# Kernel tuning notes

Hardware: AMD Instinct MI355X
Metric: run time of the kernel (lower is better)

Reference implementation:

```python
import jax, jax.numpy as jnp
import numpy as np

EPS = 1e-8


def setup_inputs() -> dict:
    key = jax.random.key(0)
    ks = jax.random.split(key, 8)
    B, N, D = 8, 2048, 768
    H, R = 768, 4
    return {
        "x": jax.random.normal(ks[0], (B, N, D), dtype=jnp.float32),
        "scale": jnp.ones((D,), dtype=jnp.float32),
        "U": jax.random.normal(ks[1], (H, R), dtype=jnp.float32) * 0.02,
        "V": jax.random.normal(ks[2], (H, R), dtype=jnp.float32) * 0.02,
        "S_param": jax.random.normal(ks[3], (H, H), dtype=jnp.float32) * 0.01,
        "Bm": jax.random.normal(ks[4], (H, D), dtype=jnp.float32) * (1.0 / np.sqrt(D)),
        "Cm": jax.random.normal(ks[5], (D, H), dtype=jnp.float32) * (1.0 / np.sqrt(H)),
        "gate_w": jax.random.normal(ks[6], (D, D), dtype=jnp.float32) * (1.0 / np.sqrt(D)),
        "gate_b": jnp.zeros((D,), dtype=jnp.float32),
        "alpha": jnp.full((1,), 0.1, dtype=jnp.float32),
    }


def reference(x, scale, U, V, S_param, Bm, Cm, gate_w, gate_b, alpha):
    B, N, D = x.shape
    H = Bm.shape[0]
    # A = diag(A_diag) + U V^T + (S - S^T); A_diag is a fixed buffer.
    A_diag = -jnp.linspace(1.0, float(H), H, dtype=x.dtype) / H
    A = jnp.diag(A_diag) + U @ V.T + (S_param - S_param.T)
    At = A.T  # apply as h @ A.T
    # RMSNorm
    rms = jnp.sqrt(jnp.mean(x * x, axis=-1, keepdims=True) + EPS)
    xn = x / rms * scale
    # Precompute input injections u_t = x_t @ B.T for all t: (N, B, H)
    u = jnp.einsum('bnd,hd->nbh', xn, Bm)

    def step(h, ut):
        h = h @ At + ut
        return h, h @ Cm.T  # (B, D)

    h0 = jnp.zeros((B, H), dtype=x.dtype)
    _, y_fwd = jax.lax.scan(step, h0, u)                 # (N, B, D)
    _, y_bwd = jax.lax.scan(step, h0, u, reverse=True)   # (N, B, D), indexed in time order
    y = 0.5 * (y_fwd + y_bwd)
    y = jnp.swapaxes(y, 0, 1)  # (B, N, D)
    # Gate
    g = jax.nn.sigmoid(jnp.einsum('bnd,ed->bne', xn, gate_w) + gate_b)
    y = y * g
    # Skip (dropout is identity in eval)
    return x + alpha * y
```

## Files before the change

kernel.cpp:

```cpp
#include <hip/hip_runtime.h>


typedef short  bfrag __attribute__((ext_vector_type(8)));
typedef float  ffrag __attribute__((ext_vector_type(4)));
typedef float  f4    __attribute__((ext_vector_type(4)));
typedef short  s4v   __attribute__((ext_vector_type(4)));

#define DEV static __device__ __forceinline__
#define Hn 768

DEV unsigned short f2bf(float f) {
  unsigned u = __float_as_uint(f);
  u += 0x7fffu + ((u >> 16) & 1u);
  return (unsigned short)(u >> 16);
}
DEV float bf2f(unsigned short s) { return __uint_as_float(((unsigned)s) << 16); }

DEV ffrag mfma16(bfrag a, bfrag b, ffrag c) {
  return __builtin_amdgcn_mfma_f32_16x16x32_bf16(a, b, c, 0, 0, 0);
}

DEV void glds16(const unsigned short* g, unsigned short* l) {
  __builtin_amdgcn_global_load_lds(
      (const __attribute__((address_space(1))) unsigned int*)g,
      (__attribute__((address_space(3))) unsigned int*)l, 16, 0, 0);
}

union BF8 { bfrag v; unsigned short u[8]; };

__global__ __launch_bounds__(256) void k_abuild(
    const float* __restrict__ U, const float* __restrict__ V,
    const float* __restrict__ S, const float* __restrict__ Bm,
    const float* __restrict__ Cm, const float* __restrict__ gw,
    float* __restrict__ Af, float* __restrict__ AfT,
    unsigned short* __restrict__ Abf,
    unsigned short* __restrict__ Bmb, unsigned short* __restrict__ Cmb,
    unsigned short* __restrict__ gwb, unsigned short* __restrict__ zp) {
  int i = blockIdx.x;
  int task = blockIdx.y;
  if (task == 0) {
    float u0 = U[i*4+0], u1 = U[i*4+1], u2 = U[i*4+2], u3 = U[i*4+3];
    for (int j = threadIdx.x; j < Hn; j += 256) {
      float a = u0*V[j*4+0] + u1*V[j*4+1] + u2*V[j*4+2] + u3*V[j*4+3]
              + S[i*Hn+j] - S[j*Hn+i];
      if (i == j) a += -(float)(i+1) / 768.0f;
      Af[i*Hn+j]  = a;
      AfT[j*Hn+i] = a;
      Abf[i*Hn+j] = f2bf(a);
    }
    if (i == 0) for (int j = threadIdx.x; j < 1024; j += 256) zp[j] = 0;
  } else {
    const float* src = (task==1) ? Bm : (task==2) ? Cm : gw;
    unsigned short* dst = (task==1) ? Bmb : (task==2) ? Cmb : gwb;
    for (int j = threadIdx.x; j < Hn; j += 256) dst[i*Hn+j] = f2bf(src[i*Hn+j]);
  }
}

__global__ __launch_bounds__(256) void k_rms(
    const float* __restrict__ x, const float* __restrict__ scale,
    unsigned short* __restrict__ xn) {
  int row  = blockIdx.x * 4 + (threadIdx.x >> 6);
  int lane = threadIdx.x & 63;
  int b = row >> 11, t = row & 2047;
  const float* xr = x + (long)row * Hn;
  float v[12];
  float ss = 0.f;
#pragma unroll
  for (int j = 0; j < 12; ++j) { v[j] = xr[lane + j*64]; ss += v[j]*v[j]; }
#pragma unroll
  for (int off = 1; off < 64; off <<= 1) ss += __shfl_xor(ss, off);
  float inv = 1.0f / sqrtf(ss / 768.0f + 1e-8f);
  unsigned short* dst = xn + ((long)t * 8 + b) * Hn;
#pragma unroll
  for (int j = 0; j < 12; ++j) dst[lane + j*64] = f2bf(v[j] * inv * scale[lane + j*64]);
}

__global__ __launch_bounds__(512) void k_sq(
    const float* __restrict__ X, const float* __restrict__ XT,
    float* __restrict__ Z, float* __restrict__ ZT,
    unsigned short* __restrict__ Zbf) {
  int tid = threadIdx.x, lane = tid & 63, w = tid >> 6;
  int mw = w >> 2, nw = w & 3, l15 = lane & 15, lhi = lane >> 4;
  int rb = blockIdx.x * 64, cb = blockIdx.y * 128;
  ffrag acc[2][2] = {};
  for (int kt = 0; kt < 24; ++kt) {
    int k0 = kt*32 + lhi*8;
    BF8 ah[2], al[2], bh[2], bl[2];
#pragma unroll
    for (int mt = 0; mt < 2; ++mt) {
      const f4* p = (const f4*)(X + (long)(rb + mw*32 + mt*16 + l15) * Hn + k0);
      f4 x0 = p[0], x1 = p[1];
#pragma unroll
      for (int j = 0; j < 8; ++j) {
        float f = (j < 4) ? x0[j] : x1[j-4];
        unsigned short h = f2bf(f);
        ah[mt].u[j] = h; al[mt].u[j] = f2bf(f - bf2f(h));
      }
    }
#pragma unroll
    for (int nt = 0; nt < 2; ++nt) {
      const f4* p = (const f4*)(XT + (long)(cb + nw*32 + nt*16 + l15) * Hn + k0);
      f4 x0 = p[0], x1 = p[1];
#pragma unroll
      for (int j = 0; j < 8; ++j) {
        float f = (j < 4) ? x0[j] : x1[j-4];
        unsigned short h = f2bf(f);
        bh[nt].u[j] = h; bl[nt].u[j] = f2bf(f - bf2f(h));
      }
    }
#pragma unroll
    for (int mt = 0; mt < 2; ++mt)
#pragma unroll
      for (int nt = 0; nt < 2; ++nt) {
        acc[mt][nt] = mfma16(ah[mt].v, bh[nt].v, acc[mt][nt]);
        acc[mt][nt] = mfma16(ah[mt].v, bl[nt].v, acc[mt][nt]);
        acc[mt][nt] = mfma16(al[mt].v, bh[nt].v, acc[mt][nt]);
      }
  }
#pragma unroll
  for (int mt = 0; mt < 2; ++mt)
#pragma unroll
    for (int nt = 0; nt < 2; ++nt)
#pragma unroll
      for (int q = 0; q < 4; ++q) {
        int grow = rb + mw*32 + mt*16 + lhi*4 + q;
        int gcol = cb + nw*32 + nt*16 + l15;
        float vv = acc[mt][nt][q];
        Z[(long)grow*Hn + gcol] = vv;
        ZT[(long)gcol*Hn + grow] = vv;
        Zbf[(long)grow*Hn + gcol] = f2bf(vv);
      }
}

template<int MODE>
__global__ __launch_bounds__(256) void k_gemm(
    const unsigned short* __restrict__ A0s, const unsigned short* __restrict__ B0s,
    const unsigned short* __restrict__ res, unsigned short* __restrict__ outb,
    const unsigned short* __restrict__ zp, int sh, int dup,
    const unsigned short* __restrict__ yb,
    const float* __restrict__ gb, const float* __restrict__ alpha,
    const float* __restrict__ x, float* __restrict__ outf) {
  constexpr int NA = (MODE == 1) ? 2 : 1;
  constexpr int NT = NA + 1;
  __shared__ unsigned short lds[2][NT * 4096];

  const int tid = threadIdx.x, lane = tid & 63, w = tid >> 6;
  const int l15 = lane & 15, lhi = lane >> 4;
  const int wr = w >> 1, wc = w & 1;

  const int nwg = gridDim.x;
  const int q8 = nwg >> 3, r8 = nwg & 7, xcd = blockIdx.x & 7, fo = blockIdx.x >> 3;
  const int wg = (xcd < r8 ? xcd*(q8+1) : r8*(q8+1) + (xcd - r8)*q8) + fo;
  const int cb = wg % 6, rbk = wg / 6;
  const long r0 = (long)rbk * 128;
  const long bc0 = (long)cb * 128;
  const int dir = (MODE == 0 && r0 >= 16384) ? 1 : 0;

  bool skip = false;
  if (MODE == 0 && sh > 0)
    skip = dir ? (r0 >= 32768 - sh) : (r0 + 128 <= sh);

  const int rowin = lane >> 2, ch = lane & 3;
  long gA[NA][2]; bool vA[NA][2]; long gB[2]; int lbase[2];
#pragma unroll
  for (int jj = 0; jj < 2; ++jj) {
    const int inst = w*2 + jj;
    const int r = inst*16 + rowin;
    const int c = ch ^ ((r ^ (r >> 2)) & 3);
    lbase[jj] = inst * 512;
#pragma unroll
    for (int s = 0; s < NA; ++s) {
      long gr; bool ok = true;
      if (MODE == 0) {
        gr = r0 + r + (dir ? sh : -sh);
        ok = dir ? (gr < 32768) : (gr >= 0);
      } else if (MODE == 1) {
        if (s == 0) { gr = r0 + r - sh; ok = (gr >= 0); }
        else        { gr = r0 + r + 16384 + sh; ok = (gr < 32768); }
      } else {
        gr = r0 + r;
      }
      vA[s][jj] = ok; gA[s][jj] = gr * Hn + c*8;
    }
    gB[jj] = (bc0 + r) * Hn + c*8;
  }

  auto stage = [&](int buf, int kt) {
    const int ko = kt * 32;
#pragma unroll
    for (int jj = 0; jj < 2; ++jj) {
#pragma unroll
      for (int s = 0; s < NA; ++s) {
        const unsigned short* g = vA[s][jj] ? (A0s + gA[s][jj] + ko) : zp;
        glds16(g, &lds[buf][s*4096 + lbase[jj]]);
      }
      glds16(B0s + gB[jj] + ko, &lds[buf][NA*4096 + lbase[jj]]);
    }
  };

  ffrag acc[4][4] = {};
  const int cx = (lhi ^ ((l15 ^ (l15 >> 2)) & 3)) * 8;

  if (!skip) {
    stage(0, 0);
    __syncthreads();
    int cur = 0;
    for (int kt = 0; kt < 24; ++kt) {
      if (kt < 23) stage(cur ^ 1, kt + 1);
      bfrag a[NA][4], b[4];
#pragma unroll
      for (int mt = 0; mt < 4; ++mt) {
        const int row = wr*64 + mt*16 + l15;
#pragma unroll
        for (int s = 0; s < NA; ++s)
          a[s][mt] = *(const bfrag*)&lds[cur][s*4096 + row*32 + cx];
      }
#pragma unroll
      for (int nt = 0; nt < 4; ++nt) {
        const int row = wc*64 + nt*16 + l15;
        b[nt] = *(const bfrag*)&lds[cur][NA*4096 + row*32 + cx];
      }
#pragma unroll
      for (int mt = 0; mt < 4; ++mt)
#pragma unroll
        for (int nt = 0; nt < 4; ++nt) {
          acc[mt][nt] = mfma16(a[0][mt], b[nt], acc[mt][nt]);
          if (NA == 2) acc[mt][nt] = mfma16(a[1][mt], b[nt], acc[mt][nt]);
        }
      __syncthreads();
      cur ^= 1;
    }
  }

  float* fl = (float*)&lds[0][0];
  const float al = (MODE == 2) ? alpha[0] : 0.f;
#pragma unroll
  for (int hh = 0; hh < 2; ++hh) {
    __syncthreads();
    if (wr == hh) {
#pragma unroll
      for (int mt = 0; mt < 4; ++mt)
#pragma unroll
        for (int nt = 0; nt < 4; ++nt)
#pragma unroll
          for (int q = 0; q < 4; ++q)
            fl[(mt*16 + lhi*4 + q)*128 + wc*64 + nt*16 + l15] = acc[mt][nt][q];
    }
    __syncthreads();
    for (int i = tid; i < 2048; i += 256) {
      const int row = i >> 5;
      const int cc  = (i & 31) << 2;
      f4 v = *(const f4*)&fl[row*128 + cc];
      const long grow = r0 + hh*64 + row;
      const long gcol = bc0 + cc;
      const long go = grow * Hn + gcol;
      if (MODE == 0) {
        if (res) {
          s4v rv = *(const s4v*)&res[go];
#pragma unroll
          for (int j = 0; j < 4; ++j) v[j] += bf2f(((unsigned short*)&rv)[j]);
        }
        s4v ov;
#pragma unroll
        for (int j = 0; j < 4; ++j) ((unsigned short*)&ov)[j] = f2bf(v[j]);
        *(s4v*)&outb[go] = ov;
        if (dup) *(s4v*)&outb[go + (long)16384*Hn] = ov;
      } else if (MODE == 1) {
        s4v ra = *(const s4v*)&res[go];
        s4v rb2 = *(const s4v*)&res[go + (long)16384*Hn];
#pragma unroll
        for (int j = 0; j < 4; ++j)
          v[j] += bf2f(((unsigned short*)&ra)[j]) + bf2f(((unsigned short*)&rb2)[j]);
        s4v ov;
#pragma unroll
        for (int j = 0; j < 4; ++j) ((unsigned short*)&ov)[j] = f2bf(v[j]);
        *(s4v*)&outb[go] = ov;
      } else {
        f4 gbv = *(const f4*)&gb[gcol];
        s4v yv = *(const s4v*)&yb[go];
        const long t = grow >> 3, b = grow & 7;
        const long o = (b*2048 + t)*Hn + gcol;
        f4 xv = *(const f4*)&x[o];
        f4 ov;
#pragma unroll
        for (int j = 0; j < 4; ++j) {
          float z = v[j] + gbv[j];
          float g = 1.0f / (1.0f + __expf(-z));
          ov[j] = xv[j] + al * 0.5f * bf2f(((unsigned short*)&yv)[j]) * g;
        }
        *(f4*)&outf[o] = ov;
      }
    }
  }
}

extern "C" void kernel_launch(void* const* d_in, const int* in_sizes, int n_in,
                              void* d_out, int out_size, void* d_ws, size_t ws_size,
                              hipStream_t stream) {
  const float* x     = (const float*)d_in[0];
  const float* scale = (const float*)d_in[1];
  const float* U     = (const float*)d_in[2];
  const float* V     = (const float*)d_in[3];
  const float* S     = (const float*)d_in[4];
  const float* Bm    = (const float*)d_in[5];
  const float* Cm    = (const float*)d_in[6];
  const float* gw    = (const float*)d_in[7];
  const float* gb    = (const float*)d_in[8];
  const float* alpha = (const float*)d_in[9];
  float* out = (float*)d_out;

  char* p = (char*)d_ws;
  auto alloc = [&](size_t sz) { char* r = p; p += (sz + 255) & ~(size_t)255; return r; };

  const size_t SZ_X  = (size_t)32768 * Hn * sizeof(unsigned short);
  const size_t SZ_BF = (size_t)16384 * Hn * sizeof(unsigned short);
  const size_t SZ_M  = (size_t)Hn * Hn * sizeof(float);
  const size_t SZ_MB = (size_t)Hn * Hn * sizeof(unsigned short);

  unsigned short* xn = (unsigned short*)alloc(SZ_BF);
  unsigned short* XA = (unsigned short*)alloc(SZ_X);
  unsigned short* XB = (unsigned short*)alloc(SZ_X);
  float* Af  = (float*)alloc(SZ_M);
  float* AfT = (float*)alloc(SZ_M);
  float* P1  = (float*)alloc(SZ_M);
  float* P1T = (float*)alloc(SZ_M);
  float* P2  = (float*)alloc(SZ_M);
  float* P2T = (float*)alloc(SZ_M);
  unsigned short* Abf = (unsigned short*)alloc(SZ_MB);
  unsigned short* Ab[10];
  for (int i = 0; i < 10; ++i) Ab[i] = (unsigned short*)alloc(SZ_MB);
  unsigned short* Bmb = (unsigned short*)alloc(SZ_MB);
  unsigned short* Cmb = (unsigned short*)alloc(SZ_MB);
  unsigned short* gwb = (unsigned short*)alloc(SZ_MB);
  unsigned short* zp  = (unsigned short*)alloc(1024 * sizeof(unsigned short));

  if ((size_t)(p - (char*)d_ws) > ws_size) return;

  k_abuild<<<dim3(768, 4), 256, 0, stream>>>(U, V, S, Bm, Cm, gw,
      Af, AfT, Abf, Bmb, Cmb, gwb, zp);
  k_rms<<<4096, 256, 0, stream>>>(x, scale, xn);

  const float* sx = Af; const float* sxt = AfT;
  float* za = P1; float* zat = P1T; float* zb = P2; float* zbt = P2T;
  for (int i = 0; i < 10; ++i) {
    k_sq<<<dim3(12, 6), 512, 0, stream>>>(sx, sxt, za, zat, Ab[i]);
    sx = za; sxt = zat;
    float* t1 = za; float* t2 = zat; za = zb; zat = zbt; zb = t1; zbt = t2;
  }

  k_gemm<0><<<768, 256, 0, stream>>>(xn, Bmb, nullptr, XA, zp, 0, 1,
      nullptr, nullptr, nullptr, nullptr, nullptr);

  unsigned short* src = XA; unsigned short* dst = XB;
  for (int i = 0; i < 10; ++i) {
    const unsigned short* W = (i == 0) ? Abf : Ab[i-1];
    k_gemm<0><<<1536, 256, 0, stream>>>(src, W, src, dst, zp, 8 << i, 0,
        nullptr, nullptr, nullptr, nullptr, nullptr);
    unsigned short* t = src; src = dst; dst = t;
  }
  k_gemm<1><<<768, 256, 0, stream>>>(src, Ab[9], src, XB, zp, 8192, 0,
      nullptr, nullptr, nullptr, nullptr, nullptr);

  unsigned short* ybuf = XB + (size_t)16384 * Hn;
  k_gemm<0><<<768, 256, 0, stream>>>(XB, Cmb, nullptr, ybuf, zp, 0, 0,
      nullptr, nullptr, nullptr, nullptr, nullptr);

  k_gemm<2><<<768, 256, 0, stream>>>(xn, gwb, nullptr, nullptr, zp, 0, 0,
      ybuf, gb, alpha, x, out);
}
```

Baseline: 1.284 ms.

## Deepen GEMM LDS pipeline to multi-buffer with vmcnt waits and pad epilogue

Replaces the double-buffered global-to-LDS staging in the bf16 MFMA GEMM with a 3- or 4-deep ring buffer. Each iteration waits with explicit s_waitcnt vmcnt counts and a single barrier, so several k-tiles of loads stay in flight. The epilogue's float staging array gets a padded row stride of 132 to reduce LDS bank conflicts. The cost is more shared memory per block, which may lower occupancy, and correctness now depends on the hand-picked vmcnt counts matching the number of loads each stage issues.

```diff
diff --git a/kernel.cpp b/kernel.cpp
--- a/kernel.cpp
+++ b/kernel.cpp
@@ -8,6 +8,7 @@
 
 #define DEV static __device__ __forceinline__
 #define Hn 768
+#define FLS 132
 
 DEV unsigned short f2bf(float f) {
   unsigned u = __float_as_uint(f);
@@ -24,6 +25,14 @@
   __builtin_amdgcn_global_load_lds(
       (const __attribute__((address_space(1))) unsigned int*)g,
       (__attribute__((address_space(3))) unsigned int*)l, 16, 0, 0);
+}
+
+template<int N> DEV void vwait() {
+  if constexpr (N == 0)       asm volatile("s_waitcnt vmcnt(0)" ::: "memory");
+  else if constexpr (N == 4)  asm volatile("s_waitcnt vmcnt(4)" ::: "memory");
+  else if constexpr (N == 6)  asm volatile("s_waitcnt vmcnt(6)" ::: "memory");
+  else if constexpr (N == 8)  asm volatile("s_waitcnt vmcnt(8)" ::: "memory");
+  else if constexpr (N == 12) asm volatile("s_waitcnt vmcnt(12)" ::: "memory");
 }
 
 union BF8 { bfrag v; unsigned short u[8]; };
@@ -140,9 +149,14 @@
     const unsigned short* __restrict__ yb,
     const float* __restrict__ gb, const float* __restrict__ alpha,
     const float* __restrict__ x, float* __restrict__ outf) {
-  constexpr int NA = (MODE == 1) ? 2 : 1;
-  constexpr int NT = NA + 1;
-  __shared__ unsigned short lds[2][NT * 4096];
+  constexpr int NA   = (MODE == 1) ? 2 : 1;
+  constexpr int NT   = NA + 1;
+  constexpr int NBUF = (MODE == 1) ? 3 : 4;
+  constexpr int LA   = NBUF - 1;
+  constexpr int NL   = 2 * NT;
+
+  __shared__ __align__(16) char smem[NBUF * NT * 8192];
+  unsigned short* ldsb = (unsigned short*)smem;
 
   const int tid = threadIdx.x, lane = tid & 63, w = tid >> 6;
   const int l15 = lane & 15, lhi = lane >> 4;
@@ -187,14 +201,15 @@
 
   auto stage = [&](int buf, int kt) {
     const int ko = kt * 32;
+    unsigned short* dst = ldsb + buf * (NT * 4096);
 #pragma unroll
     for (int jj = 0; jj < 2; ++jj) {
 #pragma unroll
       for (int s = 0; s < NA; ++s) {
         const unsigned short* g = vA[s][jj] ? (A0s + gA[s][jj] + ko) : zp;
-        glds16(g, &lds[buf][s*4096 + lbase[jj]]);
-      }
-      glds16(B0s + gB[jj] + ko, &lds[buf][NA*4096 + lbase[jj]]);
+        glds16(g, dst + s*4096 + lbase[jj]);
+      }
+      glds16(B0s + gB[jj] + ko, dst + NA*4096 + lbase[jj]);
     }
   };
 
@@ -202,23 +217,28 @@
   const int cx = (lhi ^ ((l15 ^ (l15 >> 2)) & 3)) * 8;
 
   if (!skip) {
-    stage(0, 0);
-    __syncthreads();
-    int cur = 0;
+#pragma unroll
+    for (int t = 0; t < LA; ++t) stage(t, t);
+    int cur = 0, nb = LA;
     for (int kt = 0; kt < 24; ++kt) {
-      if (kt < 23) stage(cur ^ 1, kt + 1);
+      const int rem = 23 - kt;
+      if (rem >= LA - 1) vwait<NL * (LA - 1)>();
+      else if (rem == 1) vwait<NL>();
+      else               vwait<0>();
+      __builtin_amdgcn_s_barrier();
+      const unsigned short* L = ldsb + cur * (NT * 4096);
       bfrag a[NA][4], b[4];
 #pragma unroll
       for (int mt = 0; mt < 4; ++mt) {
         const int row = wr*64 + mt*16 + l15;
 #pragma unroll
         for (int s = 0; s < NA; ++s)
-          a[s][mt] = *(const bfrag*)&lds[cur][s*4096 + row*32 + cx];
+          a[s][mt] = *(const bfrag*)&L[s*4096 + row*32 + cx];
       }
 #pragma unroll
       for (int nt = 0; nt < 4; ++nt) {
         const int row = wc*64 + nt*16 + l15;
-        b[nt] = *(const bfrag*)&lds[cur][NA*4096 + row*32 + cx];
+        b[nt] = *(const bfrag*)&L[NA*4096 + row*32 + cx];
       }
 #pragma unroll
       for (int mt = 0; mt < 4; ++mt)
@@ -227,12 +247,13 @@
           acc[mt][nt] = mfma16(a[0][mt], b[nt], acc[mt][nt]);
           if (NA == 2) acc[mt][nt] = mfma16(a[1][mt], b[nt], acc[mt][nt]);
         }
-      __syncthreads();
-      cur ^= 1;
-    }
-  }
-
-  float* fl = (float*)&lds[0][0];
+      if (kt + LA <= 23) stage(nb, kt + LA);
+      cur = (cur == NBUF-1) ? 0 : cur + 1;
+      nb  = (nb  == NBUF-1) ? 0 : nb  + 1;
+    }
+  }
+
+  float* fl = (float*)smem;
   const float al = (MODE == 2) ? alpha[0] : 0.f;
 #pragma unroll
   for (int hh = 0; hh < 2; ++hh) {
@@ -244,13 +265,13 @@
         for (int nt = 0; nt < 4; ++nt)
 #pragma unroll
           for (int q = 0; q < 4; ++q)
-            fl[(mt*16 + lhi*4 + q)*128 + wc*64 + nt*16 + l15] = acc[mt][nt][q];
+            fl[(mt*16 + lhi*4 + q)*FLS + wc*64 + nt*16 + l15] = acc[mt][nt][q];
     }
     __syncthreads();
     for (int i = tid; i < 2048; i += 256) {
       const int row = i >> 5;
       const int cc  = (i & 31) << 2;
-      f4 v = *(const f4*)&fl[row*128 + cc];
+      f4 v = *(const f4*)&fl[row*FLS + cc];
       const long grow = r0 + hh*64 + row;
       const long gcol = bc0 + cc;
       const long go = grow * Hn + gcol;
```

After: 1.311 ms. 1.02x slower.

## Use radix-4 parallel scan with three matrix powers per pass, fuse gate into output GEMM

Applied to the files above, without the earlier changes.

The linear recurrence scan becomes radix-4 instead of radix-2. Each pass multiplies by A^s, A^2s and A^3s together, which cuts the pass count from ten to five, plus a final combine step. The extra matrix powers are computed by a batched two-matrix multiply kernel. B operands are now loaded straight from global memory into registers, and the LDS bounce buffer is padded to avoid bank conflicts. The C projection and gate GEMM are fused into one kernel with a 64-row tile that applies the sigmoid gate in registers, so the y intermediate buffer is never written. The cost is more MFMA work per pass and more precomputed bf16 powers, whose rounding error may compound differently.

```diff
diff --git a/kernel.cpp b/kernel.cpp
--- a/kernel.cpp
+++ b/kernel.cpp
@@ -8,6 +8,7 @@
 
 #define DEV static __device__ __forceinline__
 #define Hn 768
+#define FLS 132
 
 DEV unsigned short f2bf(float f) {
   unsigned u = __float_as_uint(f);
@@ -75,10 +76,17 @@
   for (int j = 0; j < 12; ++j) dst[lane + j*64] = f2bf(v[j] * inv * scale[lane + j*64]);
 }
 
-__global__ __launch_bounds__(512) void k_sq(
-    const float* __restrict__ X, const float* __restrict__ XT,
-    float* __restrict__ Z, float* __restrict__ ZT,
-    unsigned short* __restrict__ Zbf) {
+__global__ __launch_bounds__(512) void k_mul(
+    const float* __restrict__ X0, const float* __restrict__ Y0T,
+    float* __restrict__ Z0, float* __restrict__ Z0T, unsigned short* __restrict__ Zb0,
+    const float* __restrict__ X1, const float* __restrict__ Y1T,
+    float* __restrict__ Z1, float* __restrict__ Z1T, unsigned short* __restrict__ Zb1) {
+  const float* X  = blockIdx.z ? X1 : X0;
+  const float* YT = blockIdx.z ? Y1T : Y0T;
+  float* Z  = blockIdx.z ? Z1 : Z0;
+  float* ZT = blockIdx.z ? Z1T : Z0T;
+  unsigned short* Zb = blockIdx.z ? Zb1 : Zb0;
+
   int tid = threadIdx.x, lane = tid & 63, w = tid >> 6;
   int mw = w >> 2, nw = w & 3, l15 = lane & 15, lhi = lane >> 4;
   int rb = blockIdx.x * 64, cb = blockIdx.y * 128;
@@ -99,7 +107,7 @@
     }
 #pragma unroll
     for (int nt = 0; nt < 2; ++nt) {
-      const f4* p = (const f4*)(XT + (long)(cb + nw*32 + nt*16 + l15) * Hn + k0);
+      const f4* p = (const f4*)(YT + (long)(cb + nw*32 + nt*16 + l15) * Hn + k0);
       f4 x0 = p[0], x1 = p[1];
 #pragma unroll
       for (int j = 0; j < 8; ++j) {
@@ -126,23 +134,31 @@
         int grow = rb + mw*32 + mt*16 + lhi*4 + q;
         int gcol = cb + nw*32 + nt*16 + l15;
         float vv = acc[mt][nt][q];
-        Z[(long)grow*Hn + gcol] = vv;
-        ZT[(long)gcol*Hn + grow] = vv;
-        Zbf[(long)grow*Hn + gcol] = f2bf(vv);
+        if (Z)  Z[(long)grow*Hn + gcol] = vv;
+        if (ZT) ZT[(long)gcol*Hn + grow] = vv;
+        Zb[(long)grow*Hn + gcol] = f2bf(vv);
       }
 }
 
 template<int MODE>
 __global__ __launch_bounds__(256) void k_gemm(
-    const unsigned short* __restrict__ A0s, const unsigned short* __restrict__ B0s,
+    const unsigned short* __restrict__ A0s, const unsigned short* __restrict__ A1s,
+    const unsigned short* __restrict__ B0s, const unsigned short* __restrict__ B1s,
+    const unsigned short* __restrict__ B2s,
     const unsigned short* __restrict__ res, unsigned short* __restrict__ outb,
-    const unsigned short* __restrict__ zp, int sh, int dup,
-    const unsigned short* __restrict__ yb,
+    const unsigned short* __restrict__ zp, int sh,
     const float* __restrict__ gb, const float* __restrict__ alpha,
     const float* __restrict__ x, float* __restrict__ outf) {
-  constexpr int NA = (MODE == 1) ? 2 : 1;
-  constexpr int NT = NA + 1;
-  __shared__ unsigned short lds[2][NT * 4096];
+  constexpr int NS   = (MODE == 0) ? 1 : (MODE == 1) ? 3 : 2;
+  constexpr int MT   = (MODE == 3) ? 2 : 4;
+  constexpr int ROWS = MT * 32;
+  constexpr int NJ   = ROWS / 64;
+  constexpr int TILE = ROWS * 32;
+  constexpr size_t STG = (size_t)2 * NS * TILE * 2;
+  constexpr size_t BNC = (size_t)(MT * 16) * FLS * 4;
+  constexpr size_t LB  = STG > BNC ? STG : BNC;
+  __shared__ __align__(16) char smem[LB];
+  unsigned short* ldsb = (unsigned short*)smem;
 
   const int tid = threadIdx.x, lane = tid & 63, w = tid >> 6;
   const int l15 = lane & 15, lhi = lane >> 4;
@@ -152,120 +168,150 @@
   const int q8 = nwg >> 3, r8 = nwg & 7, xcd = blockIdx.x & 7, fo = blockIdx.x >> 3;
   const int wg = (xcd < r8 ? xcd*(q8+1) : r8*(q8+1) + (xcd - r8)*q8) + fo;
   const int cb = wg % 6, rbk = wg / 6;
-  const long r0 = (long)rbk * 128;
+  const long r0 = (long)rbk * ROWS;
   const long bc0 = (long)cb * 128;
-  const int dir = (MODE == 0 && r0 >= 16384) ? 1 : 0;
+  const int dir = (MODE == 1 && r0 >= 16384) ? 1 : 0;
 
   bool skip = false;
-  if (MODE == 0 && sh > 0)
-    skip = dir ? (r0 >= 32768 - sh) : (r0 + 128 <= sh);
+  if (MODE == 1)
+    skip = dir ? (r0 >= 32768 - sh) : (r0 + ROWS <= sh);
 
   const int rowin = lane >> 2, ch = lane & 3;
-  long gA[NA][2]; bool vA[NA][2]; long gB[2]; int lbase[2];
-#pragma unroll
-  for (int jj = 0; jj < 2; ++jj) {
-    const int inst = w*2 + jj;
+  long gA[NS][NJ]; bool vA[NS][NJ]; int lbase[NJ];
+#pragma unroll
+  for (int jj = 0; jj < NJ; ++jj) {
+    const int inst = w*NJ + jj;
     const int r = inst*16 + rowin;
     const int c = ch ^ ((r ^ (r >> 2)) & 3);
     lbase[jj] = inst * 512;
 #pragma unroll
-    for (int s = 0; s < NA; ++s) {
+    for (int s = 0; s < NS; ++s) {
       long gr; bool ok = true;
-      if (MODE == 0) {
-        gr = r0 + r + (dir ? sh : -sh);
+      if (MODE == 0 || MODE == 3) {
+        gr = r0 + r;
+      } else if (MODE == 1) {
+        gr = r0 + r + (dir ? (s+1)*sh : -(s+1)*sh);
         ok = dir ? (gr < 32768) : (gr >= 0);
-      } else if (MODE == 1) {
-        if (s == 0) { gr = r0 + r - sh; ok = (gr >= 0); }
-        else        { gr = r0 + r + 16384 + sh; ok = (gr < 32768); }
       } else {
-        gr = r0 + r;
+        if (s == 0) { gr = r0 + r - sh;          ok = (gr >= 0);    }
+        else        { gr = r0 + r + 16384 + sh;  ok = (gr < 32768); }
       }
       vA[s][jj] = ok; gA[s][jj] = gr * Hn + c*8;
     }
-    gB[jj] = (bc0 + r) * Hn + c*8;
   }
 
   auto stage = [&](int buf, int kt) {
     const int ko = kt * 32;
-#pragma unroll
-    for (int jj = 0; jj < 2; ++jj) {
-#pragma unroll
-      for (int s = 0; s < NA; ++s) {
-        const unsigned short* g = vA[s][jj] ? (A0s + gA[s][jj] + ko) : zp;
-        glds16(g, &lds[buf][s*4096 + lbase[jj]]);
-      }
-      glds16(B0s + gB[jj] + ko, &lds[buf][NA*4096 + lbase[jj]]);
-    }
+    unsigned short* dst = ldsb + buf * (NS * TILE);
+#pragma unroll
+    for (int jj = 0; jj < NJ; ++jj)
+#pragma unroll
+      for (int s = 0; s < NS; ++s) {
+        const unsigned short* src = (MODE == 3 && s == 1) ? A1s : A0s;
+        const unsigned short* g = vA[s][jj] ? (src + gA[s][jj] + ko) : zp;
+        glds16(g, dst + s*TILE + lbase[jj]);
+      }
   };
 
-  ffrag acc[4][4] = {};
+  ffrag acc[MT][4] = {};
+  ffrag accZ[(MODE == 3) ? 2 : 1][(MODE == 3) ? 4 : 1] = {};
   const int cx = (lhi ^ ((l15 ^ (l15 >> 2)) & 3)) * 8;
+
+  auto bld = [&](const unsigned short* W, int kt, int nt) {
+    return *(const bfrag*)(W + (long)(bc0 + wc*64 + nt*16 + l15) * Hn
+                             + kt*32 + lhi*8);
+  };
 
   if (!skip) {
     stage(0, 0);
     __syncthreads();
     int cur = 0;
     for (int kt = 0; kt < 24; ++kt) {
+      bfrag ball[NS][4];
+#pragma unroll
+      for (int s = 0; s < NS; ++s) {
+        const unsigned short* W =
+            (MODE == 2) ? B0s : (s == 0) ? B0s : (s == 1) ? B1s : B2s;
+#pragma unroll
+        for (int nt = 0; nt < 4; ++nt) ball[s][nt] = bld(W, kt, nt);
+      }
       if (kt < 23) stage(cur ^ 1, kt + 1);
-      bfrag a[NA][4], b[4];
-#pragma unroll
-      for (int mt = 0; mt < 4; ++mt) {
-        const int row = wr*64 + mt*16 + l15;
-#pragma unroll
-        for (int s = 0; s < NA; ++s)
-          a[s][mt] = *(const bfrag*)&lds[cur][s*4096 + row*32 + cx];
-      }
-#pragma unroll
-      for (int nt = 0; nt < 4; ++nt) {
-        const int row = wc*64 + nt*16 + l15;
-        b[nt] = *(const bfrag*)&lds[cur][NA*4096 + row*32 + cx];
-      }
-#pragma unroll
-      for (int mt = 0; mt < 4; ++mt)
-#pragma unroll
-        for (int nt = 0; nt < 4; ++nt) {
-          acc[mt][nt] = mfma16(a[0][mt], b[nt], acc[mt][nt]);
-          if (NA == 2) acc[mt][nt] = mfma16(a[1][mt], b[nt], acc[mt][nt]);
-        }
+      const unsigned short* L = ldsb + cur * (NS * TILE);
+#pragma unroll
+      for (int s = 0; s < NS; ++s) {
+        bfrag a[MT];
+#pragma unroll
+        for (int mt = 0; mt < MT; ++mt)
+          a[mt] = *(const bfrag*)&L[s*TILE + (wr*(MT*16) + mt*16 + l15)*32 + cx];
+#pragma unroll
+        for (int mt = 0; mt < MT; ++mt)
+#pragma unroll
+          for (int nt = 0; nt < 4; ++nt) {
+            if (MODE == 3 && s == 1)
+              accZ[mt][nt] = mfma16(a[mt], ball[s][nt], accZ[mt][nt]);
+            else
+              acc[mt][nt] = mfma16(a[mt], ball[s][nt], acc[mt][nt]);
+          }
+      }
       __syncthreads();
       cur ^= 1;
     }
   }
 
-  float* fl = (float*)&lds[0][0];
-  const float al = (MODE == 2) ? alpha[0] : 0.f;
+  if (MODE == 3) {
+    const float al = alpha[0];
+    float gvals[4];
+#pragma unroll
+    for (int nt = 0; nt < 4; ++nt) gvals[nt] = gb[bc0 + wc*64 + nt*16 + l15];
+#pragma unroll
+    for (int mt = 0; mt < MT; ++mt)
+#pragma unroll
+      for (int nt = 0; nt < 4; ++nt)
+#pragma unroll
+        for (int q = 0; q < 4; ++q) {
+          float z = accZ[mt][nt][q] + gvals[nt];
+          float g = 1.0f / (1.0f + __expf(-z));
+          acc[mt][nt][q] *= al * 0.5f * g;
+        }
+  }
+
+  constexpr int HR = MT * 16;
+  float* fl = (float*)smem;
 #pragma unroll
   for (int hh = 0; hh < 2; ++hh) {
     __syncthreads();
     if (wr == hh) {
 #pragma unroll
-      for (int mt = 0; mt < 4; ++mt)
+      for (int mt = 0; mt < MT; ++mt)
 #pragma unroll
         for (int nt = 0; nt < 4; ++nt)
 #pragma unroll
           for (int q = 0; q < 4; ++q)
-            fl[(mt*16 + lhi*4 + q)*128 + wc*64 + nt*16 + l15] = acc[mt][nt][q];
+            fl[(mt*16 + lhi*4 + q)*FLS + wc*64 + nt*16 + l15] = acc[mt][nt][q];
     }
     __syncthreads();
-    for (int i = tid; i < 2048; i += 256) {
+    for (int i = tid; i < HR*32; i += 256) {
       const int row = i >> 5;
       const int cc  = (i & 31) << 2;
-      f4 v = *(const f4*)&fl[row*128 + cc];
-      const long grow = r0 + hh*64 + row;
+      f4 v = *(const f4*)&fl[row*FLS + cc];
+      const long grow = r0 + hh*HR + row;
       const long gcol = bc0 + cc;
       const long go = grow * Hn + gcol;
       if (MODE == 0) {
-        if (res) {
-          s4v rv = *(const s4v*)&res[go];
-#pragma unroll
-          for (int j = 0; j < 4; ++j) v[j] += bf2f(((unsigned short*)&rv)[j]);
-        }
         s4v ov;
 #pragma unroll
         for (int j = 0; j < 4; ++j) ((unsigned short*)&ov)[j] = f2bf(v[j]);
         *(s4v*)&outb[go] = ov;
-        if (dup) *(s4v*)&outb[go + (long)16384*Hn] = ov;
+        *(s4v*)&outb[go + (long)16384*Hn] = ov;
       } else if (MODE == 1) {
+        s4v rv = *(const s4v*)&res[go];
+#pragma unroll
+        for (int j = 0; j < 4; ++j) v[j] += bf2f(((unsigned short*)&rv)[j]);
+        s4v ov;
+#pragma unroll
+        for (int j = 0; j < 4; ++j) ((unsigned short*)&ov)[j] = f2bf(v[j]);
+        *(s4v*)&outb[go] = ov;
+      } else if (MODE == 2) {
         s4v ra = *(const s4v*)&res[go];
         s4v rb2 = *(const s4v*)&res[go + (long)16384*Hn];
 #pragma unroll
@@ -276,18 +322,12 @@
         for (int j = 0; j < 4; ++j) ((unsigned short*)&ov)[j] = f2bf(v[j]);
         *(s4v*)&outb[go] = ov;
       } else {
-        f4 gbv = *(const f4*)&gb[gcol];
-        s4v yv = *(const s4v*)&yb[go];
         const long t = grow >> 3, b = grow & 7;
         const long o = (b*2048 + t)*Hn + gcol;
         f4 xv = *(const f4*)&x[o];
         f4 ov;
 #pragma unroll
-        for (int j = 0; j < 4; ++j) {
-          float z = v[j] + gbv[j];
-          float g = 1.0f / (1.0f + __expf(-z));
-          ov[j] = xv[j] + al * 0.5f * bf2f(((unsigned short*)&yv)[j]) * g;
-        }
+        for (int j = 0; j < 4; ++j) ov[j] = xv[j] + v[j];
         *(f4*)&outf[o] = ov;
       }
     }
@@ -322,13 +362,15 @@
   unsigned short* XB = (unsigned short*)alloc(SZ_X);
   float* Af  = (float*)alloc(SZ_M);
   float* AfT = (float*)alloc(SZ_M);
-  float* P1  = (float*)alloc(SZ_M);
-  float* P1T = (float*)alloc(SZ_M);
-  float* P2  = (float*)alloc(SZ_M);
-  float* P2T = (float*)alloc(SZ_M);
+  float* K0  = (float*)alloc(SZ_M);  float* K0T = (float*)alloc(SZ_M);
+  float* K1  = (float*)alloc(SZ_M);  float* K1T = (float*)alloc(SZ_M);
+  float* K2  = (float*)alloc(SZ_M);  float* K2T = (float*)alloc(SZ_M);
   unsigned short* Abf = (unsigned short*)alloc(SZ_MB);
-  unsigned short* Ab[10];
-  for (int i = 0; i < 10; ++i) Ab[i] = (unsigned short*)alloc(SZ_MB);
+  unsigned short* Pb[15];
+  for (int i = 0; i < 15; ++i) Pb[i] = (unsigned short*)alloc(SZ_MB);
+  unsigned short* A2b=Pb[0],*A3b=Pb[1],*A4b=Pb[2],*A8b=Pb[3],*A12b=Pb[4],
+      *A16b=Pb[5],*A32b=Pb[6],*A48b=Pb[7],*A64b=Pb[8],*A128b=Pb[9],
+      *A192b=Pb[10],*A256b=Pb[11],*A512b=Pb[12],*A768b=Pb[13],*A1024b=Pb[14];
   unsigned short* Bmb = (unsigned short*)alloc(SZ_MB);
   unsigned short* Cmb = (unsigned short*)alloc(SZ_MB);
   unsigned short* gwb = (unsigned short*)alloc(SZ_MB);
@@ -340,31 +382,45 @@
       Af, AfT, Abf, Bmb, Cmb, gwb, zp);
   k_rms<<<4096, 256, 0, stream>>>(x, scale, xn);
 
-  const float* sx = Af; const float* sxt = AfT;
-  float* za = P1; float* zat = P1T; float* zb = P2; float* zbt = P2T;
-  for (int i = 0; i < 10; ++i) {
-    k_sq<<<dim3(12, 6), 512, 0, stream>>>(sx, sxt, za, zat, Ab[i]);
-    sx = za; sxt = zat;
-    float* t1 = za; float* t2 = zat; za = zb; zat = zbt; zb = t1; zbt = t2;
-  }
-
-  k_gemm<0><<<768, 256, 0, stream>>>(xn, Bmb, nullptr, XA, zp, 0, 1,
-      nullptr, nullptr, nullptr, nullptr, nullptr);
-
-  unsigned short* src = XA; unsigned short* dst = XB;
-  for (int i = 0; i < 10; ++i) {
-    const unsigned short* W = (i == 0) ? Abf : Ab[i-1];
-    k_gemm<0><<<1536, 256, 0, stream>>>(src, W, src, dst, zp, 8 << i, 0,
-        nullptr, nullptr, nullptr, nullptr, nullptr);
-    unsigned short* t = src; src = dst; dst = t;
-  }
-  k_gemm<1><<<768, 256, 0, stream>>>(src, Ab[9], src, XB, zp, 8192, 0,
-      nullptr, nullptr, nullptr, nullptr, nullptr);
-
-  unsigned short* ybuf = XB + (size_t)16384 * Hn;
-  k_gemm<0><<<768, 256, 0, stream>>>(XB, Cmb, nullptr, ybuf, zp, 0, 0,
-      nullptr, nullptr, nullptr, nullptr, nullptr);
-
-  k_gemm<2><<<768, 256, 0, stream>>>(xn, gwb, nullptr, nullptr, zp, 0, 0,
-      ybuf, gb, alpha, x, out);
-}
+  dim3 g1(12, 6, 1), g2(12, 6, 2);
+  k_mul<<<g1, 512, 0, stream>>>(Af, AfT, K0, K0T, A2b,
+                                nullptr, nullptr, nullptr, nullptr, nullptr);
+  k_mul<<<g2, 512, 0, stream>>>(Af, K0T, nullptr, nullptr, A3b,
+                                K0, K0T, K1, K1T, A4b);
+  k_mul<<<g1, 512, 0, stream>>>(K1, K1T, K2, K2T, A8b,
+                                nullptr, nullptr, nullptr, nullptr, nullptr);
+  k_mul<<<g2, 512, 0, stream>>>(K1, K2T, nullptr, nullptr, A12b,
+                                K2, K2T, K0, K0T, A16b);
+  k_mul<<<g1, 512, 0, stream>>>(K0, K0T, K1, K1T, A32b,
+                                nullptr, nullptr, nullptr, nullptr, nullptr);
+  k_mul<<<g2, 512, 0, stream>>>(K0, K1T, nullptr, nullptr, A48b,
+                                K1, K1T, K2, K2T, A64b);
+  k_mul<<<g1, 512, 0, stream>>>(K2, K2T, K0, K0T, A128b,
+                                nullptr, nullptr, nullptr, nullptr, nullptr);
+  k_mul<<<g2, 512, 0, stream>>>(K2, K0T, nullptr, nullptr, A192b,
+                                K0, K0T, K1, K1T, A256b);
+  k_mul<<<g1, 512, 0, stream>>>(K1, K1T, K2, K2T, A512b,
+                                nullptr, nullptr, nullptr, nullptr, nullptr);
+  k_mul<<<g2, 512, 0, stream>>>(K1, K2T, nullptr, nullptr, A768b,
+                                K2, K2T, nullptr, nullptr, A1024b);
+
+  k_gemm<0><<<768, 256, 0, stream>>>(xn, nullptr, Bmb, nullptr, nullptr,
+      nullptr, XA, zp, 0, nullptr, nullptr, nullptr, nullptr);
+
+  k_gemm<1><<<1536, 256, 0, stream>>>(XA, nullptr, Abf,  A2b,  A3b,
+      XA, XB, zp, 8,    nullptr, nullptr, nullptr, nullptr);
+  k_gemm<1><<<1536, 256, 0, stream>>>(XB, nullptr, A4b,  A8b,  A12b,
+      XB, XA, zp, 32,   nullptr, nullptr, nullptr, nullptr);
+  k_gemm<1><<<1536, 256, 0, stream>>>(XA, nullptr, A16b, A32b, A48b,
+      XA, XB, zp, 128,  nullptr, nullptr, nullptr, nullptr);
+  k_gemm<1><<<1536, 256, 0, stream>>>(XB, nullptr, A64b, A128b, A192b,
+      XB, XA, zp, 512,  nullptr, nullptr, nullptr, nullptr);
+  k_gemm<1><<<1536, 256, 0, stream>>>(XA, nullptr, A256b, A512b, A768b,
+      XA, XB, zp, 2048, nullptr, nullptr, nullptr, nullptr);
+
+  k_gemm<2><<<768, 256, 0, stream>>>(XB, nullptr, A1024b, nullptr, nullptr,
+      XB, XA, zp, 8192, nullptr, nullptr, nullptr, nullptr);
+
+  k_gemm<3><<<1536, 256, 0, stream>>>(XA, xn, Cmb, gwb, nullptr,
+      nullptr, nullptr, zp, 0, gb, alpha, x, out);
+}
```

New measurement: 2.050 ms. +59.7%, slower.
